# Performance work log

Hardware: AMD Instinct MI355X
Metric: run time of the kernel (lower is better)

Reference implementation:

```python
import jax, jax.numpy as jnp
import numpy as np

NUM_EXPERTS = 8
D_IN = 4096
D_OUT = 4096


def setup_inputs() -> dict:
    key = jax.random.key(0)
    k_x, k_gw, k_gb, k_ew, k_eb = jax.random.split(key, 5)
    x = jax.random.normal(k_x, (4, 2048, D_IN), dtype=jnp.float32)
    gate_w = jax.random.normal(k_gw, (NUM_EXPERTS, D_IN), dtype=jnp.float32) * 0.02
    gate_b = jax.random.normal(k_gb, (NUM_EXPERTS,), dtype=jnp.float32) * 0.02
    expert_w = jax.random.normal(k_ew, (NUM_EXPERTS, D_OUT, D_IN), dtype=jnp.float32) * 0.02
    expert_b = jax.random.normal(k_eb, (NUM_EXPERTS, D_OUT), dtype=jnp.float32) * 0.02
    return {"x": x, "gate_w": gate_w, "gate_b": gate_b,
            "expert_w": expert_w, "expert_b": expert_b}


def reference(x, gate_w, gate_b, expert_w, expert_b):
    # Flatten tokens: [T, D_IN]
    orig_shape = x.shape
    xf = x.reshape(-1, x.shape[-1])
    # Gating: softmax over logits, then top-1 (argmax of softmax == argmax of logits)
    gate_logits = xf @ gate_w.T + gate_b            # [T, E]
    gates = jax.nn.softmax(gate_logits, axis=-1)
    selected = jnp.argmax(gates, axis=-1)           # [T] int
    # Per-expert Linear applied to the tokens routed to it (dense-masked grouped GEMM).
    # Faithful to the module: top-1 dispatch, no gate-probability weighting of output.
    out = jnp.zeros((xf.shape[0], expert_w.shape[1]), dtype=xf.dtype)
    for j in range(expert_w.shape[0]):  # fixed small expert count
        yj = xf @ expert_w[j].T + expert_b[j]       # [T, D_OUT]
        out = out + jnp.where((selected == j)[:, None], yj, 0.0)
    return out.reshape(*orig_shape[:-1], expert_w.shape[1])
```

## Files before the change

kernel.cpp:

```cpp
#include <hip/hip_runtime.h>

#define NE   8
#define DIN  4096
#define DOUT 4096
#define TOK  8192

#define BM 128
#define BN 128
#define BK 32
#define NT (DIN / BK)
#define BUFE (BM * BK)

#define FBM 128
#define FBK 32
#define LDSK 40

typedef __attribute__((ext_vector_type(4))) float f32x4;
typedef __attribute__((ext_vector_type(8))) short bf16x8;
typedef __attribute__((ext_vector_type(2))) unsigned long long u64x2;

#define AS1 __attribute__((address_space(1)))
#define AS3 __attribute__((address_space(3)))

static __device__ __forceinline__ unsigned short f2bf(float f) {
  unsigned u = __builtin_bit_cast(unsigned, f);
  u += 0x7fffu + ((u >> 16) & 1u);
  return (unsigned short)(u >> 16);
}

static __device__ __forceinline__ unsigned long long pack4(f32x4 v) {
  return (unsigned long long)f2bf(v[0])
       | ((unsigned long long)f2bf(v[1]) << 16)
       | ((unsigned long long)f2bf(v[2]) << 32)
       | ((unsigned long long)f2bf(v[3]) << 48);
}

static __device__ __forceinline__ void gload16(const void* g, void* l) {
  __builtin_amdgcn_global_load_lds((const AS1 unsigned int*)g,
                                   (AS3 unsigned int*)l, 16, 0, 0);
}

__global__ void prep_kernel(const float* __restrict__ x, const float* __restrict__ gw,
                            const float* __restrict__ gb, int* __restrict__ counts,
                            int* __restrict__ tlist, unsigned short* __restrict__ xbf,
                            const float* __restrict__ ew, unsigned short* __restrict__ wbf) {
  if (blockIdx.x < TOK / 4) {
    const int lane = threadIdx.x & 63;
    const int tok  = blockIdx.x * 4 + (threadIdx.x >> 6);
    const float* xr = x + (size_t)tok * DIN;
    unsigned short* xo = xbf + (size_t)tok * DIN;
    float acc[NE];
    #pragma unroll
    for (int e = 0; e < NE; ++e) acc[e] = 0.f;
    for (int i = lane * 4; i < DIN; i += 256) {
      f32x4 xv = *(const f32x4*)(xr + i);
      *(unsigned long long*)(xo + i) = pack4(xv);
      #pragma unroll
      for (int e = 0; e < NE; ++e) {
        f32x4 wv = *(const f32x4*)(gw + e * DIN + i);
        acc[e] += xv[0]*wv[0] + xv[1]*wv[1] + xv[2]*wv[2] + xv[3]*wv[3];
      }
    }
    #pragma unroll
    for (int e = 0; e < NE; ++e) {
      float v = acc[e];
      #pragma unroll
      for (int o = 32; o > 0; o >>= 1) v += __shfl_xor(v, o);
      acc[e] = v;
    }
    if (lane == 0) {
      float bv = acc[0] + gb[0];
      int best = 0;
      #pragma unroll
      for (int e = 1; e < NE; ++e) {
        float v = acc[e] + gb[e];
        if (v > bv) { bv = v; best = e; }
      }
      int pos = atomicAdd(&counts[best], 1);
      tlist[best * TOK + pos] = tok;
    }
  } else {
    const int bid = blockIdx.x - TOK / 4;
    const size_t n = (size_t)NE * DOUT * DIN;
    size_t idx = ((size_t)bid * 256 + threadIdx.x) * 8;
    const size_t stride = (size_t)8192 * 256 * 8;
    for (; idx < n; idx += stride) {
      f32x4 a = *(const f32x4*)(ew + idx);
      f32x4 b = *(const f32x4*)(ew + idx + 4);
      u64x2 v; v[0] = pack4(a); v[1] = pack4(b);
      *(u64x2*)(wbf + idx) = v;
    }
  }
}

__global__ __launch_bounds__(256, 3)
void moe_gemm_bf(const unsigned short* __restrict__ xbf,
                 const unsigned short* __restrict__ wbf,
                 const float* __restrict__ eb,
                 const int* __restrict__ counts,
                 const int* __restrict__ tlist,
                 float* __restrict__ out) {
  __shared__ unsigned short sA[3][BUFE];
  __shared__ unsigned short sB[3][BUFE];
  __shared__ int rowtok[BM];

  const int tid = threadIdx.x;

  const int cpx  = gridDim.x >> 3;
  const int wgid = ((int)blockIdx.x & 7) * cpx + ((int)blockIdx.x >> 3);
  const int ntile = wgid & 31;
  const int slot  = wgid >> 5;

  int e = -1, mtile = 0, Me = 0;
  {
    int accn = 0;
    #pragma unroll
    for (int j = 0; j < NE; ++j) {
      int c = counts[j];
      int tt = (c + BM - 1) / BM;
      if (e < 0 && slot < accn + tt) { e = j; mtile = slot - accn; Me = c; }
      accn += tt;
    }
  }
  if (e < 0) return;

  const int n0 = ntile * BN;
  const int m0 = mtile * BM;
  const unsigned short* wbase = wbf + (size_t)e * DOUT * DIN;

  if (tid < BM) {
    int r = m0 + tid;
    rowtok[tid] = tlist[e * TOK + (r < Me ? r : Me - 1)];
  }
  __syncthreads();

  const int w = tid >> 6, l = tid & 63;

  const int srow  = tid >> 2;
  const int sslot = tid & 3;
  const int colsw = (sslot ^ ((srow >> 2) & 3)) * 8;

  const unsigned short* ga0 = xbf   + (size_t)rowtok[srow]      * DIN + colsw;
  const unsigned short* ga1 = xbf   + (size_t)rowtok[srow + 64] * DIN + colsw;
  const unsigned short* gb0 = wbase + (size_t)(n0 + srow)       * DIN + colsw;
  const unsigned short* gb1 = wbase + (size_t)(n0 + srow + 64)  * DIN + colsw;
  const int ldsb = w * 512;

  const int wr = (w >> 1) * 64;
  const int wc = (w & 1) * 64;
  const int lr = l & 15, lk = l >> 4;
  int offA[4], offB[4];
  #pragma unroll
  for (int m = 0; m < 4; ++m) {
    int r = wr + m * 16 + lr;
    offA[m] = r * BK + ((lk ^ ((r >> 2) & 3)) * 8);
  }
  #pragma unroll
  for (int n = 0; n < 4; ++n) {
    int r = wc + n * 16 + lr;
    offB[n] = r * BK + ((lk ^ ((r >> 2) & 3)) * 8);
  }

  f32x4 acc[4][4];
  #pragma unroll
  for (int m = 0; m < 4; ++m)
    #pragma unroll
    for (int n = 0; n < 4; ++n) acc[m][n] = (f32x4){0.f, 0.f, 0.f, 0.f};

#define STAGE(kt, b) do {                                   \
    const int ko_ = (kt) * BK;                              \
    gload16(ga0 + ko_, &sA[b][ldsb]);                       \
    gload16(ga1 + ko_, &sA[b][2048 + ldsb]);                \
    gload16(gb0 + ko_, &sB[b][ldsb]);                       \
    gload16(gb1 + ko_, &sB[b][2048 + ldsb]);                \
  } while (0)

  STAGE(0, 0);
  STAGE(1, 1);
  asm volatile("s_waitcnt vmcnt(4)" ::: "memory");
  __builtin_amdgcn_s_barrier();
  asm volatile("" ::: "memory");

  int bc = 0, bs = 2;
  for (int t = 0; t < NT; ++t) {
    const int ts = (t + 2 < NT) ? t + 2 : NT - 1;
    STAGE(ts, bs);

    bf16x8 av[4], bv[4];
    #pragma unroll
    for (int m = 0; m < 4; ++m) av[m] = *(const bf16x8*)&sA[bc][offA[m]];
    #pragma unroll
    for (int n = 0; n < 4; ++n) bv[n] = *(const bf16x8*)&sB[bc][offB[n]];

    __builtin_amdgcn_s_setprio(1);
    #pragma unroll
    for (int m = 0; m < 4; ++m)
      #pragma unroll
      for (int n = 0; n < 4; ++n)
        acc[m][n] = __builtin_amdgcn_mfma_f32_16x16x32_bf16(av[m], bv[n], acc[m][n], 0, 0, 0);
    __builtin_amdgcn_s_setprio(0);

    asm volatile("s_waitcnt vmcnt(4)" ::: "memory");
    __builtin_amdgcn_s_barrier();
    asm volatile("" ::: "memory");

    bc = (bc == 2) ? 0 : bc + 1;
    bs = (bs == 2) ? 0 : bs + 1;
  }

  float bias[4];
  #pragma unroll
  for (int n = 0; n < 4; ++n) bias[n] = eb[e * DOUT + n0 + wc + n * 16 + lr];

  #pragma unroll
  for (int m = 0; m < 4; ++m) {
    #pragma unroll
    for (int j = 0; j < 4; ++j) {
      int rloc = wr + m * 16 + lk * 4 + j;
      if (m0 + rloc < Me) {
        int tokr = rowtok[rloc];
        float* op = out + (size_t)tokr * DOUT + n0 + wc;
        #pragma unroll
        for (int n = 0; n < 4; ++n)
          op[n * 16 + lr] = acc[m][n][j] + bias[n];
      }
    }
  }
#undef STAGE
}

__global__ void gate_kernel(const float* __restrict__ x, const float* __restrict__ gw,
                            const float* __restrict__ gb, int* __restrict__ counts,
                            int* __restrict__ tlist) {
  const int lane = threadIdx.x & 63;
  const int tok  = blockIdx.x * 4 + (threadIdx.x >> 6);
  const float* xr = x + (size_t)tok * DIN;
  float acc[NE];
  #pragma unroll
  for (int e = 0; e < NE; ++e) acc[e] = 0.f;
  for (int i = lane; i < DIN; i += 64) {
    float xv = xr[i];
    #pragma unroll
    for (int e = 0; e < NE; ++e) acc[e] += xv * gw[e * DIN + i];
  }
  #pragma unroll
  for (int e = 0; e < NE; ++e) {
    float v = acc[e];
    #pragma unroll
    for (int o = 32; o > 0; o >>= 1) v += __shfl_xor(v, o);
    acc[e] = v;
  }
  if (lane == 0) {
    float bv = acc[0] + gb[0];
    int best = 0;
    #pragma unroll
    for (int e = 1; e < NE; ++e) {
      float v = acc[e] + gb[e];
      if (v > bv) { bv = v; best = e; }
    }
    int pos = atomicAdd(&counts[best], 1);
    tlist[best * TOK + pos] = tok;
  }
}

__global__ __launch_bounds__(256, 2)
void moe_gemm(const float* __restrict__ x, const float* __restrict__ ew,
              const float* __restrict__ eb, const int* __restrict__ counts,
              const int* __restrict__ tlist, float* __restrict__ out) {
  __shared__ unsigned short fA[2][FBM * LDSK];
  __shared__ unsigned short fB[2][FBM * LDSK];
  __shared__ int rowtok[FBM];

  const int tid  = threadIdx.x;
  const int slot = blockIdx.y;

  int e = -1, mtile = 0, Me = 0;
  {
    int acc = 0;
    #pragma unroll
    for (int j = 0; j < NE; ++j) {
      int c = counts[j];
      int t = (c + FBM - 1) / FBM;
      if (e < 0 && slot < acc + t) { e = j; mtile = slot - acc; Me = c; }
      acc += t;
    }
  }
  if (e < 0) return;

  const int n0 = blockIdx.x * FBM;
  const int m0 = mtile * FBM;
  const float* we = ew + (size_t)e * DOUT * DIN;

  if (tid < FBM) {
    int r = m0 + tid;
    rowtok[tid] = tlist[e * TOK + (r < Me ? r : Me - 1)];
  }
  __syncthreads();

  const int srow = tid >> 3;
  const int scol = (tid & 7) * 4;
  const int lane = tid & 63;
  const int w  = tid >> 6;
  const int wr = (w >> 1) * 64;
  const int wc = (w & 1) * 64;
  const int lr = lane & 15;
  const int lk = lane >> 4;

  f32x4 accf[4][4];
  #pragma unroll
  for (int m = 0; m < 4; ++m)
    #pragma unroll
    for (int n = 0; n < 4; ++n) accf[m][n] = (f32x4){0.f, 0.f, 0.f, 0.f};

  const float* aptr[4];
  const float* bptr[4];
  #pragma unroll
  for (int p = 0; p < 4; ++p) {
    int r = p * 32 + srow;
    aptr[p] = x  + (size_t)rowtok[r] * DIN + scol;
    bptr[p] = we + (size_t)(n0 + r)  * DIN + scol;
  }

  #pragma unroll
  for (int p = 0; p < 4; ++p) {
    int r = p * 32 + srow;
    *(unsigned long long*)&fA[0][r * LDSK + scol] = pack4(*(const f32x4*)(aptr[p]));
    *(unsigned long long*)&fB[0][r * LDSK + scol] = pack4(*(const f32x4*)(bptr[p]));
  }
  __syncthreads();

  int cur = 0;
  for (int kt = 0; kt < DIN / FBK; ++kt) {
    f32x4 ra[4], rb[4];
    const bool more = (kt + 1 < DIN / FBK);
    if (more) {
      const int koff = (kt + 1) * FBK;
      #pragma unroll
      for (int p = 0; p < 4; ++p) {
        ra[p] = *(const f32x4*)(aptr[p] + koff);
        rb[p] = *(const f32x4*)(bptr[p] + koff);
      }
    }
    bf16x8 af[4], bfr[4];
    #pragma unroll
    for (int m = 0; m < 4; ++m)
      af[m] = *(const bf16x8*)&fA[cur][(wr + m * 16 + lr) * LDSK + lk * 8];
    #pragma unroll
    for (int n = 0; n < 4; ++n)
      bfr[n] = *(const bf16x8*)&fB[cur][(wc + n * 16 + lr) * LDSK + lk * 8];
    #pragma unroll
    for (int m = 0; m < 4; ++m)
      #pragma unroll
      for (int n = 0; n < 4; ++n)
        accf[m][n] = __builtin_amdgcn_mfma_f32_16x16x32_bf16(af[m], bfr[n], accf[m][n], 0, 0, 0);
    if (more) {
      #pragma unroll
      for (int p = 0; p < 4; ++p) {
        int r = p * 32 + srow;
        *(unsigned long long*)&fA[cur ^ 1][r * LDSK + scol] = pack4(ra[p]);
        *(unsigned long long*)&fB[cur ^ 1][r * LDSK + scol] = pack4(rb[p]);
      }
    }
    __syncthreads();
    cur ^= 1;
  }

  float bias[4];
  #pragma unroll
  for (int n = 0; n < 4; ++n) bias[n] = eb[e * DOUT + n0 + wc + n * 16 + lr];

  #pragma unroll
  for (int m = 0; m < 4; ++m) {
    #pragma unroll
    for (int j = 0; j < 4; ++j) {
      int rloc = wr + m * 16 + lk * 4 + j;
      if (m0 + rloc < Me) {
        int tokr = rowtok[rloc];
        float* op = out + (size_t)tokr * DOUT + n0 + wc;
        #pragma unroll
        for (int n = 0; n < 4; ++n)
          op[n * 16 + lr] = accf[m][n][j] + bias[n];
      }
    }
  }
}

extern "C" void kernel_launch(void* const* d_in, const int* in_sizes, int n_in,
                              void* d_out, int out_size, void* d_ws, size_t ws_size,
                              hipStream_t stream) {
  const float* x  = (const float*)d_in[0];
  const float* gw = (const float*)d_in[1];
  const float* gb = (const float*)d_in[2];
  const float* ew = (const float*)d_in[3];
  const float* eb = (const float*)d_in[4];
  float* out = (float*)d_out;

  int* counts = (int*)d_ws;
  int* tlist  = counts + 16;
  const size_t XOFF = 1u << 20;
  const size_t WOFF = XOFF + (size_t)TOK * DIN * 2;
  const size_t NEED = WOFF + (size_t)NE * DOUT * DIN * 2;

  hipMemsetAsync(counts, 0, 16 * sizeof(int), stream);

  if (ws_size >= NEED) {
    unsigned short* xbf = (unsigned short*)((char*)d_ws + XOFF);
    unsigned short* wbf = (unsigned short*)((char*)d_ws + WOFF);
    prep_kernel<<<TOK / 4 + 8192, 256, 0, stream>>>(x, gw, gb, counts, tlist, xbf, ew, wbf);
    moe_gemm_bf<<<32 * (TOK / BM + NE), 256, 0, stream>>>(xbf, wbf, eb, counts, tlist, out);
  } else {
    gate_kernel<<<TOK / 4, 256, 0, stream>>>(x, gw, gb, counts, tlist);
    dim3 grid(DOUT / FBM, TOK / FBM + NE, 1);
    moe_gemm<<<grid, 256, 0, stream>>>(x, ew, eb, counts, tlist, out);
  }
}
```

Baseline: 671.6 us.

## Enlarge bf16 GEMM tile to 256x128x64 with 512 threads and split-phase pipeline

The bf16 expert GEMM now uses 256-row M tiles, a K step of 64 and 8 waves per block. LDS is one flat triple buffer with an XOR swizzle over 8 column groups. Each K step is split into two phases, and the global loads for A and B of the step two ahead are issued between the LDS reads and the MFMAs, separated by barriers. The aim is more operand reuse per byte loaded and fewer barriers per unit of work. In exchange it uses more LDS (about 144KB for two blocks per CU), pads more rows at expert tile boundaries, and leaves fewer blocks in the grid.

```diff
diff --git a/kernel.cpp b/kernel.cpp
--- a/kernel.cpp
+++ b/kernel.cpp
@@ -5,14 +5,13 @@
 #define DOUT 4096
 #define TOK  8192
 
-#define BM 128
+#define BM 256
 #define BN 128
+#define BKF 64
+#define NKT (DIN / BKF)
+#define BUFE 24576
+
 #define BK 32
-#define NT (DIN / BK)
-#define BUFE (BM * BK)
-
-#define FBM 128
-#define FBK 32
 #define LDSK 40
 
 typedef __attribute__((ext_vector_type(4))) float f32x4;
@@ -93,15 +92,14 @@
   }
 }
 
-__global__ __launch_bounds__(256, 3)
+__global__ __launch_bounds__(512, 2)
 void moe_gemm_bf(const unsigned short* __restrict__ xbf,
                  const unsigned short* __restrict__ wbf,
                  const float* __restrict__ eb,
                  const int* __restrict__ counts,
                  const int* __restrict__ tlist,
                  float* __restrict__ out) {
-  __shared__ unsigned short sA[3][BUFE];
-  __shared__ unsigned short sB[3][BUFE];
+  __shared__ unsigned short lds[3 * BUFE];
   __shared__ int rowtok[BM];
 
   const int tid = threadIdx.x;
@@ -136,97 +134,98 @@
 
   const int w = tid >> 6, l = tid & 63;
 
-  const int srow  = tid >> 2;
-  const int sslot = tid & 3;
-  const int colsw = (sslot ^ ((srow >> 2) & 3)) * 8;
-
-  const unsigned short* ga0 = xbf   + (size_t)rowtok[srow]      * DIN + colsw;
-  const unsigned short* ga1 = xbf   + (size_t)rowtok[srow + 64] * DIN + colsw;
-  const unsigned short* gb0 = wbase + (size_t)(n0 + srow)       * DIN + colsw;
-  const unsigned short* gb1 = wbase + (size_t)(n0 + srow + 64)  * DIN + colsw;
-  const int ldsb = w * 512;
-
-  const int wr = (w >> 1) * 64;
-  const int wc = (w & 1) * 64;
-  const int lr = l & 15, lk = l >> 4;
+  const int srow = tid >> 3, sj = tid & 7;
+  const int colsw = (sj ^ (srow & 7)) * 8;
+  const unsigned short* pa0 = xbf + (size_t)rowtok[srow]       * DIN + colsw;
+  const unsigned short* pa1 = xbf + (size_t)rowtok[srow + 64]  * DIN + colsw;
+  const unsigned short* pa2 = xbf + (size_t)rowtok[srow + 128] * DIN + colsw;
+  const unsigned short* pa3 = xbf + (size_t)rowtok[srow + 192] * DIN + colsw;
+  const unsigned short* pb0 = wbase + (size_t)(n0 + srow)      * DIN + colsw;
+  const unsigned short* pb1 = wbase + (size_t)(n0 + srow + 64) * DIN + colsw;
+  const int dw = w << 9;
+
+  const int wm = w >> 1, wn = w & 1;
+  const int lr = l & 15, lk = l >> 4, lr7 = l & 7;
   int offA[4], offB[4];
   #pragma unroll
-  for (int m = 0; m < 4; ++m) {
-    int r = wr + m * 16 + lr;
-    offA[m] = r * BK + ((lk ^ ((r >> 2) & 3)) * 8);
-  }
-  #pragma unroll
-  for (int n = 0; n < 4; ++n) {
-    int r = wc + n * 16 + lr;
-    offB[n] = r * BK + ((lk ^ ((r >> 2) & 3)) * 8);
-  }
+  for (int mi = 0; mi < 4; ++mi) offA[mi] = (wm * 64 + mi * 16 + lr) * BKF;
+  #pragma unroll
+  for (int ni = 0; ni < 4; ++ni) offB[ni] = 16384 + (wn * 64 + ni * 16 + lr) * BKF;
 
   f32x4 acc[4][4];
   #pragma unroll
-  for (int m = 0; m < 4; ++m)
-    #pragma unroll
-    for (int n = 0; n < 4; ++n) acc[m][n] = (f32x4){0.f, 0.f, 0.f, 0.f};
-
-#define STAGE(kt, b) do {                                   \
-    const int ko_ = (kt) * BK;                              \
-    gload16(ga0 + ko_, &sA[b][ldsb]);                       \
-    gload16(ga1 + ko_, &sA[b][2048 + ldsb]);                \
-    gload16(gb0 + ko_, &sB[b][ldsb]);                       \
-    gload16(gb1 + ko_, &sB[b][2048 + ldsb]);                \
+  for (int mi = 0; mi < 4; ++mi)
+    #pragma unroll
+    for (int ni = 0; ni < 4; ++ni) acc[mi][ni] = (f32x4){0.f, 0.f, 0.f, 0.f};
+
+#define STAGE_A(gk, b) do { const int ko_ = (gk) * BKF;                       \
+    const int d_ = (b) * BUFE + dw;                                           \
+    gload16(pa0 + ko_, &lds[d_]);                                             \
+    gload16(pa1 + ko_, &lds[d_ + 4096]);                                      \
+    gload16(pa2 + ko_, &lds[d_ + 8192]);                                      \
+    gload16(pa3 + ko_, &lds[d_ + 12288]); } while (0)
+#define STAGE_B(gk, b) do { const int ko_ = (gk) * BKF;                       \
+    const int d_ = (b) * BUFE + 16384 + dw;                                   \
+    gload16(pb0 + ko_, &lds[d_]);                                             \
+    gload16(pb1 + ko_, &lds[d_ + 4096]); } while (0)
+#define PHASE(base, ks, STAGE_STMT) do {                                      \
+    const int so_ = (((ks) * 4 + lk) ^ lr7) * 8;                              \
+    bf16x8 av[4], bv[4];                                                      \
+    _Pragma("unroll") for (int mi = 0; mi < 4; ++mi)                          \
+      av[mi] = *(const bf16x8*)&lds[(base) + offA[mi] + so_];                 \
+    _Pragma("unroll") for (int ni = 0; ni < 4; ++ni)                          \
+      bv[ni] = *(const bf16x8*)&lds[(base) + offB[ni] + so_];                 \
+    STAGE_STMT;                                                               \
+    asm volatile("" ::: "memory");                                            \
+    __builtin_amdgcn_s_barrier();                                             \
+    asm volatile("" ::: "memory");                                            \
+    __builtin_amdgcn_s_setprio(1);                                            \
+    _Pragma("unroll") for (int mi = 0; mi < 4; ++mi)                          \
+      _Pragma("unroll") for (int ni = 0; ni < 4; ++ni)                        \
+        acc[mi][ni] = __builtin_amdgcn_mfma_f32_16x16x32_bf16(av[mi], bv[ni], acc[mi][ni], 0, 0, 0); \
+    __builtin_amdgcn_s_setprio(0);                                            \
+    asm volatile("" ::: "memory");                                            \
+    __builtin_amdgcn_s_barrier();                                             \
+    asm volatile("" ::: "memory");                                            \
   } while (0)
 
-  STAGE(0, 0);
-  STAGE(1, 1);
-  asm volatile("s_waitcnt vmcnt(4)" ::: "memory");
-  __builtin_amdgcn_s_barrier();
-  asm volatile("" ::: "memory");
-
-  int bc = 0, bs = 2;
-  for (int t = 0; t < NT; ++t) {
-    const int ts = (t + 2 < NT) ? t + 2 : NT - 1;
-    STAGE(ts, bs);
-
-    bf16x8 av[4], bv[4];
-    #pragma unroll
-    for (int m = 0; m < 4; ++m) av[m] = *(const bf16x8*)&sA[bc][offA[m]];
-    #pragma unroll
-    for (int n = 0; n < 4; ++n) bv[n] = *(const bf16x8*)&sB[bc][offB[n]];
-
-    __builtin_amdgcn_s_setprio(1);
-    #pragma unroll
-    for (int m = 0; m < 4; ++m)
-      #pragma unroll
-      for (int n = 0; n < 4; ++n)
-        acc[m][n] = __builtin_amdgcn_mfma_f32_16x16x32_bf16(av[m], bv[n], acc[m][n], 0, 0, 0);
-    __builtin_amdgcn_s_setprio(0);
-
-    asm volatile("s_waitcnt vmcnt(4)" ::: "memory");
+  STAGE_A(0, 0); STAGE_B(0, 0);
+  STAGE_A(1, 1); STAGE_B(1, 1);
+
+  int bR = 0, bS = 2;
+  for (int g = 0; g < NKT; ++g) {
+    const int gk2 = (g + 2 < NKT) ? g + 2 : NKT - 1;
+    asm volatile("s_waitcnt vmcnt(6)" ::: "memory");
     __builtin_amdgcn_s_barrier();
     asm volatile("" ::: "memory");
-
-    bc = (bc == 2) ? 0 : bc + 1;
-    bs = (bs == 2) ? 0 : bs + 1;
+    const int base = bR * BUFE;
+    PHASE(base, 0, STAGE_A(gk2, bS));
+    PHASE(base, 1, STAGE_B(gk2, bS));
+    bR = (bR == 2) ? 0 : bR + 1;
+    bS = (bS == 2) ? 0 : bS + 1;
   }
 
   float bias[4];
   #pragma unroll
-  for (int n = 0; n < 4; ++n) bias[n] = eb[e * DOUT + n0 + wc + n * 16 + lr];
-
-  #pragma unroll
-  for (int m = 0; m < 4; ++m) {
+  for (int ni = 0; ni < 4; ++ni) bias[ni] = eb[e * DOUT + n0 + wn * 64 + ni * 16 + lr];
+
+  #pragma unroll
+  for (int mi = 0; mi < 4; ++mi) {
     #pragma unroll
     for (int j = 0; j < 4; ++j) {
-      int rloc = wr + m * 16 + lk * 4 + j;
+      int rloc = wm * 64 + mi * 16 + lk * 4 + j;
       if (m0 + rloc < Me) {
         int tokr = rowtok[rloc];
-        float* op = out + (size_t)tokr * DOUT + n0 + wc;
+        float* op = out + (size_t)tokr * DOUT + n0 + wn * 64;
         #pragma unroll
-        for (int n = 0; n < 4; ++n)
-          op[n * 16 + lr] = acc[m][n][j] + bias[n];
-      }
-    }
-  }
-#undef STAGE
+        for (int ni = 0; ni < 4; ++ni)
+          op[ni * 16 + lr] = acc[mi][ni][j] + bias[ni];
+      }
+    }
+  }
+#undef STAGE_A
+#undef STAGE_B
+#undef PHASE
 }
 
 __global__ void gate_kernel(const float* __restrict__ x, const float* __restrict__ gw,
@@ -267,9 +266,9 @@
 void moe_gemm(const float* __restrict__ x, const float* __restrict__ ew,
               const float* __restrict__ eb, const int* __restrict__ counts,
               const int* __restrict__ tlist, float* __restrict__ out) {
-  __shared__ unsigned short fA[2][FBM * LDSK];
-  __shared__ unsigned short fB[2][FBM * LDSK];
-  __shared__ int rowtok[FBM];
+  __shared__ unsigned short fA[2][128 * LDSK];
+  __shared__ unsigned short fB[2][128 * LDSK];
+  __shared__ int rowtok[128];
 
   const int tid  = threadIdx.x;
   const int slot = blockIdx.y;
@@ -280,18 +279,18 @@
     #pragma unroll
     for (int j = 0; j < NE; ++j) {
       int c = counts[j];
-      int t = (c + FBM - 1) / FBM;
+      int t = (c + 127) / 128;
       if (e < 0 && slot < acc + t) { e = j; mtile = slot - acc; Me = c; }
       acc += t;
     }
   }
   if (e < 0) return;
 
-  const int n0 = blockIdx.x * FBM;
-  const int m0 = mtile * FBM;
+  const int n0 = blockIdx.x * 128;
+  const int m0 = mtile * 128;
   const float* we = ew + (size_t)e * DOUT * DIN;
 
-  if (tid < FBM) {
+  if (tid < 128) {
     int r = m0 + tid;
     rowtok[tid] = tlist[e * TOK + (r < Me ? r : Me - 1)];
   }
@@ -330,11 +329,11 @@
   __syncthreads();
 
   int cur = 0;
-  for (int kt = 0; kt < DIN / FBK; ++kt) {
+  for (int kt = 0; kt < DIN / BK; ++kt) {
     f32x4 ra[4], rb[4];
-    const bool more = (kt + 1 < DIN / FBK);
+    const bool more = (kt + 1 < DIN / BK);
     if (more) {
-      const int koff = (kt + 1) * FBK;
+      const int koff = (kt + 1) * BK;
       #pragma unroll
       for (int p = 0; p < 4; ++p) {
         ra[p] = *(const f32x4*)(aptr[p] + koff);
@@ -407,10 +406,10 @@
     unsigned short* xbf = (unsigned short*)((char*)d_ws + XOFF);
     unsigned short* wbf = (unsigned short*)((char*)d_ws + WOFF);
     prep_kernel<<<TOK / 4 + 8192, 256, 0, stream>>>(x, gw, gb, counts, tlist, xbf, ew, wbf);
-    moe_gemm_bf<<<32 * (TOK / BM + NE), 256, 0, stream>>>(xbf, wbf, eb, counts, tlist, out);
+    moe_gemm_bf<<<32 * (TOK / BM + NE), 512, 0, stream>>>(xbf, wbf, eb, counts, tlist, out);
   } else {
     gate_kernel<<<TOK / 4, 256, 0, stream>>>(x, gw, gb, counts, tlist);
-    dim3 grid(DOUT / FBM, TOK / FBM + NE, 1);
+    dim3 grid(DOUT / 128, TOK / 128 + NE, 1);
     moe_gemm<<<grid, 256, 0, stream>>>(x, ew, eb, counts, tlist, out);
   }
 }
```

Result: slower. 718.1 us (+6.9%).
